# Optimization experiments

Hardware: AMD Instinct MI355X
Metric: run time of the kernel (lower is better)

The kernel has to match this reference:

```python
import jax, jax.numpy as jnp
import numpy as np

B, F, D = 32, 4096, 256
ALPHA = 0.001


def setup_inputs() -> dict:
    key = jax.random.key(0)
    ks = jax.random.split(key, 9)
    s = 1.0 / np.sqrt(D)
    return {
        "q": jax.random.normal(ks[0], (B, F, D), dtype=jnp.float32),
        "k": jax.random.normal(ks[1], (B, F, D), dtype=jnp.float32),
        "v": jax.random.normal(ks[2], (B, F, D), dtype=jnp.float32),
        "Wq": jax.random.normal(ks[3], (D, D), dtype=jnp.float32) * s,
        "bq": jax.random.normal(ks[4], (D,), dtype=jnp.float32) * 0.01,
        "Wk": jax.random.normal(ks[5], (D, D), dtype=jnp.float32) * s,
        "bk": jax.random.normal(ks[6], (D,), dtype=jnp.float32) * 0.01,
        "Wv": jax.random.normal(ks[7], (D, D), dtype=jnp.float32) * s,
        "bv": jax.random.normal(ks[8], (D,), dtype=jnp.float32) * 0.01,
    }


def reference(q, k, v, Wq, bq, Wk, bk, Wv, bv):
    # nn.Linear: x @ W.T + b
    queries = q @ Wq.T + bq            # [b, f, d]
    keys = k @ Wk.T + bk               # [b, f, d]
    values = v @ Wv.T + bv             # [b, f, d]
    # batched Gram matrix + ridge term
    key_sym = jnp.einsum("bfd,bfe->bde", keys, keys)          # [b, d, d]
    key_sym = key_sym + ALPHA * jnp.eye(D, dtype=key_sym.dtype)
    key_sym_inv = jnp.linalg.inv(key_sym)                      # [b, d, d]
    kkik = jnp.einsum("bde,bfe->bdf", key_sym_inv, keys)       # [b, d, f]
    kkikv = jnp.einsum("bdf,bfe->bde", kkik, values)           # [b, d, d]
    itn = jax.nn.softmax(kkikv, axis=2)                        # sigma=True; softmax over dim 2
    h = jnp.einsum("bfd,bde->be", queries, itn)                # [b, d]
    return h
```

## Files before the change

### kernel.cpp

```cpp
#include <hip/hip_runtime.h>
#include <math.h>

#define FDIM 4096
#define DDIM 256
#define ALPHA_R 0.001f
#define SVH (3 * 32 * 256)

typedef __attribute__((ext_vector_type(8))) short short8;
typedef __attribute__((ext_vector_type(4))) float f32x4;

__device__ __forceinline__ unsigned cvt_pk_bf16(float lo_e, float hi_e) {
  unsigned r;
  asm("v_cvt_pk_bf16_f32 %0, %1, %2" : "=v"(r) : "v"(lo_e), "v"(hi_e));
  return r;
}

__global__ __launch_bounds__(256) void gram_fused(const float* __restrict__ kg,
                                                  const float* __restrict__ vg,
                                                  const float* __restrict__ qg,
                                                  float* __restrict__ Gp0,
                                                  float* __restrict__ Gp1,
                                                  float* __restrict__ svec,
                                                  float* __restrict__ part) {
  int flat = blockIdx.x;
  int tid = threadIdx.x;

  if (flat >= 1024) {
    int cs = flat - 1024;
    int chunk = cs & 15, b = cs >> 4;
    int rg = tid >> 6, dq = tid & 63;
    const float* p = qg + ((size_t)b * FDIM + chunk * 256 + rg) * DDIM + dq * 4;
    float4 s = make_float4(0.f, 0.f, 0.f, 0.f);
    for (int i = 0; i < 64; ++i) {
      float4 t = *(const float4*)(p + (size_t)i * 4 * DDIM);
      s.x += t.x; s.y += t.y; s.z += t.z; s.w += t.w;
    }
    __shared__ __align__(16) float redq[4][64][4];
    *(float4*)&redq[rg][dq][0] = s;
    __syncthreads();
    if (rg == 0) {
      float4 a0 = *(float4*)&redq[0][dq][0];
      float4 a1 = *(float4*)&redq[1][dq][0];
      float4 a2 = *(float4*)&redq[2][dq][0];
      float4 a3 = *(float4*)&redq[3][dq][0];
      float4 t = make_float4(a0.x + a1.x + a2.x + a3.x, a0.y + a1.y + a2.y + a3.y,
                             a0.z + a1.z + a2.z + a3.z, a0.w + a1.w + a2.w + a3.w);
      *(float4*)(part + ((size_t)chunk * 32 + b) * DDIM + dq * 4) = t;
    }
    return;
  }

  int xcd = flat & 7, s = flat >> 3;
  int b = xcd * 4 + (s >> 5);
  int rem = s & 31;
  int tile = rem >> 1;
  int half = rem & 1;
  int tm = tile >> 2, tn = tile & 3;
  int mBase = tm * 64, nBase = tn * 64;
  const float* Kb = kg + (size_t)b * FDIM * DDIM;
  const float* Vb = vg + (size_t)b * FDIM * DDIM;

  __shared__ __align__(16) unsigned short Ah[64][40], Al[64][40];
  __shared__ __align__(16) unsigned short Bh[64][40], Bl[64][40];
  __shared__ __align__(16) unsigned short Ch[64][40], Cl[64][40];
  __shared__ float sred[4][68];

  int w = tid >> 6, lane = tid & 63;
  int wr = w >> 1, wc = w & 1;
  int lrow = lane & 15;
  int kof = (lane >> 4) * 8;

  const float* pA = Kb + mBase + lane;
  const float* pB = Kb + nBase + lane;
  const float* pC = Vb + nBase + lane;

  bool doK = (tn == 0), doV = (tm == 0);
  float sK = 0.f, sV = 0.f;
  int fBase = half * 2048;

  float xa[8], xb[8], xc[8];
  auto loadIter = [&](int it) {
    int f = fBase + it * 32 + w * 8;
#pragma unroll
    for (int j = 0; j < 8; ++j) {
      xa[j] = pA[(size_t)(f + j) * DDIM];
      xb[j] = pB[(size_t)(f + j) * DDIM];
      xc[j] = pC[(size_t)(f + j) * DDIM];
    }
  };
  auto stash = [&](const float* x, unsigned short (*H)[40], unsigned short (*L)[40]) {
    unsigned h0 = cvt_pk_bf16(x[0], x[1]);
    unsigned h1 = cvt_pk_bf16(x[2], x[3]);
    unsigned h2 = cvt_pk_bf16(x[4], x[5]);
    unsigned h3 = cvt_pk_bf16(x[6], x[7]);
    unsigned l0 = cvt_pk_bf16(x[0] - __uint_as_float(h0 << 16),
                              x[1] - __uint_as_float(h0 & 0xFFFF0000u));
    unsigned l1 = cvt_pk_bf16(x[2] - __uint_as_float(h1 << 16),
                              x[3] - __uint_as_float(h1 & 0xFFFF0000u));
    unsigned l2 = cvt_pk_bf16(x[4] - __uint_as_float(h2 << 16),
                              x[5] - __uint_as_float(h2 & 0xFFFF0000u));
    unsigned l3 = cvt_pk_bf16(x[6] - __uint_as_float(h3 << 16),
                              x[7] - __uint_as_float(h3 & 0xFFFF0000u));
    *(uint4*)&H[lane][w * 8] = make_uint4(h0, h1, h2, h3);
    *(uint4*)&L[lane][w * 8] = make_uint4(l0, l1, l2, l3);
  };

  f32x4 acc0[2][2], acc1[2][2];
#pragma unroll
  for (int mt = 0; mt < 2; ++mt)
#pragma unroll
    for (int nt = 0; nt < 2; ++nt) {
      acc0[mt][nt] = (f32x4){0.f, 0.f, 0.f, 0.f};
      acc1[mt][nt] = (f32x4){0.f, 0.f, 0.f, 0.f};
    }

  loadIter(0);
  for (int it = 0; it < 64; ++it) {
    __syncthreads();
    stash(xa, Ah, Al);
    stash(xb, Bh, Bl);
    stash(xc, Ch, Cl);
    if (doK) sK += ((xa[0] + xa[1]) + (xa[2] + xa[3])) + ((xa[4] + xa[5]) + (xa[6] + xa[7]));
    if (doV) sV += ((xc[0] + xc[1]) + (xc[2] + xc[3])) + ((xc[4] + xc[5]) + (xc[6] + xc[7]));
    __syncthreads();
    if (it < 63) loadIter(it + 1);

    short8 bh[2], bl[2], ch[2], cl[2];
#pragma unroll
    for (int nt = 0; nt < 2; ++nt) {
      int rB = wc * 32 + nt * 16 + lrow;
      bh[nt] = *(const short8*)&Bh[rB][kof];
      bl[nt] = *(const short8*)&Bl[rB][kof];
      ch[nt] = *(const short8*)&Ch[rB][kof];
      cl[nt] = *(const short8*)&Cl[rB][kof];
    }
    __builtin_amdgcn_s_setprio(1);
#pragma unroll
    for (int mt = 0; mt < 2; ++mt) {
      int rA = wr * 32 + mt * 16 + lrow;
      short8 ah = *(const short8*)&Ah[rA][kof];
      short8 al = *(const short8*)&Al[rA][kof];
#pragma unroll
      for (int nt = 0; nt < 2; ++nt) {
        f32x4 t = acc0[mt][nt];
        t = __builtin_amdgcn_mfma_f32_16x16x32_bf16(ah, bh[nt], t, 0, 0, 0);
        t = __builtin_amdgcn_mfma_f32_16x16x32_bf16(ah, bl[nt], t, 0, 0, 0);
        t = __builtin_amdgcn_mfma_f32_16x16x32_bf16(al, bh[nt], t, 0, 0, 0);
        acc0[mt][nt] = t;
        f32x4 u = acc1[mt][nt];
        u = __builtin_amdgcn_mfma_f32_16x16x32_bf16(ah, ch[nt], u, 0, 0, 0);
        u = __builtin_amdgcn_mfma_f32_16x16x32_bf16(ah, cl[nt], u, 0, 0, 0);
        u = __builtin_amdgcn_mfma_f32_16x16x32_bf16(al, ch[nt], u, 0, 0, 0);
        acc1[mt][nt] = u;
      }
    }
    __builtin_amdgcn_s_setprio(0);
  }

  float* Gp = half ? Gp1 : Gp0;
  float* G0 = Gp + ((size_t)b * 2) * 65536;
  float* G1 = G0 + 65536;
#pragma unroll
  for (int mt = 0; mt < 2; ++mt)
#pragma unroll
    for (int nt = 0; nt < 2; ++nt)
#pragma unroll
      for (int r = 0; r < 4; ++r) {
        int row = mBase + wr * 32 + mt * 16 + (lane >> 4) * 4 + r;
        int col = nBase + wc * 32 + nt * 16 + (lane & 15);
        G0[(size_t)row * DDIM + col] = acc0[mt][nt][r];
        G1[(size_t)row * DDIM + col] = acc1[mt][nt][r];
      }

  float* svecH = svec + (size_t)half * SVH;
  if (doK) {
    __syncthreads();
    sred[w][lane] = sK;
    __syncthreads();
    if (tid < 64) {
      float t = sred[0][tid] + sred[1][tid] + sred[2][tid] + sred[3][tid];
      svecH[(size_t)1 * 32 * 256 + (size_t)b * 256 + mBase + tid] = t;
    }
  }
  if (doV) {
    __syncthreads();
    sred[w][lane] = sV;
    __syncthreads();
    if (tid < 64) {
      float t = sred[0][tid] + sred[1][tid] + sred[2][tid] + sred[3][tid];
      svecH[(size_t)2 * 32 * 256 + (size_t)b * 256 + nBase + tid] = t;
    }
  }
}

__global__ void smallvec(const float* __restrict__ Wq, const float* __restrict__ bq,
                         const float* __restrict__ Wk, const float* __restrict__ Wv,
                         const float* __restrict__ part,
                         const float* __restrict__ svec, float* __restrict__ uvec) {
  int b = blockIdx.x; int d = threadIdx.x;
  __shared__ float sq[256], sk[256], sv[256];
  float sqv = 0.f;
  for (int c = 0; c < 16; ++c) sqv += part[((size_t)c * 32 + b) * DDIM + d];
  sq[d] = sqv;
  sk[d] = svec[((size_t)1 * 32 + b) * DDIM + d] + svec[SVH + ((size_t)1 * 32 + b) * DDIM + d];
  sv[d] = svec[((size_t)2 * 32 + b) * DDIM + d] + svec[SVH + ((size_t)2 * 32 + b) * DDIM + d];
  __syncthreads();
  float uk = 0.f, uv = 0.f, uq = 0.f;
  for (int j = 0; j < 256; j += 4) {
    float4 wk4 = *(const float4*)(Wk + (size_t)d * DDIM + j);
    float4 wv4 = *(const float4*)(Wv + (size_t)d * DDIM + j);
    float4 wq4 = *(const float4*)(Wq + (size_t)d * DDIM + j);
    uk += wk4.x * sk[j] + wk4.y * sk[j + 1] + wk4.z * sk[j + 2] + wk4.w * sk[j + 3];
    uv += wv4.x * sv[j] + wv4.y * sv[j + 1] + wv4.z * sv[j + 2] + wv4.w * sv[j + 3];
    uq += wq4.x * sq[j] + wq4.y * sq[j + 1] + wq4.z * sq[j + 2] + wq4.w * sq[j + 3];
  }
  uvec[((size_t)0 * 32 + b) * DDIM + d] = uk;
  uvec[((size_t)1 * 32 + b) * DDIM + d] = uv;
  uvec[((size_t)2 * 32 + b) * DDIM + d] = uq + 4096.f * bq[d];
}

__global__ __launch_bounds__(256) void gemm_pass1(const float* __restrict__ Wk,
                                                  const float* __restrict__ Gp0,
                                                  const float* __restrict__ Gp1,
                                                  float* __restrict__ T) {
  int tile = blockIdx.x, w = blockIdx.y, b = blockIdx.z;
  int tm = tile >> 2, tn = tile & 3;
  const float* A = Wk;
  const float* B0 = Gp0 + ((size_t)b * 2 + w) * 65536;
  const float* B1 = Gp1 + ((size_t)b * 2 + w) * 65536;
  float* C = T + ((size_t)b * 2 + w) * 65536;
  __shared__ __align__(16) float As[16][64];
  __shared__ __align__(16) float Bs[16][64];
  int tid = threadIdx.x;
  int ty = tid >> 4, tx = tid & 15;
  int am = tid & 63, ak4 = tid >> 6;
  int brow = tid >> 4, bcol4 = tid & 15;
  int mBase = tm * 64, nBase = tn * 64;
  float acc[4][4];
#pragma unroll
  for (int i = 0; i < 4; i++)
#pragma unroll
    for (int j = 0; j < 4; j++) acc[i][j] = 0.f;
  for (int k0 = 0; k0 < 256; k0 += 16) {
    float4 a = *(const float4*)(A + (size_t)(mBase + am) * DDIM + k0 + ak4 * 4);
    size_t boff = (size_t)(k0 + brow) * DDIM + nBase + bcol4 * 4;
    float4 b0 = *(const float4*)(B0 + boff);
    float4 b1 = *(const float4*)(B1 + boff);
    float4 bb = make_float4(b0.x + b1.x, b0.y + b1.y, b0.z + b1.z, b0.w + b1.w);
    __syncthreads();
    As[ak4 * 4 + 0][am] = a.x; As[ak4 * 4 + 1][am] = a.y;
    As[ak4 * 4 + 2][am] = a.z; As[ak4 * 4 + 3][am] = a.w;
    *(float4*)&Bs[brow][bcol4 * 4] = bb;
    __syncthreads();
#pragma unroll
    for (int kstep = 0; kstep < 16; ++kstep) {
      float4 a4 = *(const float4*)&As[kstep][ty * 4];
      float4 b4 = *(const float4*)&Bs[kstep][tx * 4];
      float av[4] = {a4.x, a4.y, a4.z, a4.w};
      float bvv[4] = {b4.x, b4.y, b4.z, b4.w};
#pragma unroll
      for (int i = 0; i < 4; i++)
#pragma unroll
        for (int j = 0; j < 4; j++)
          acc[i][j] = fmaf(av[i], bvv[j], acc[i][j]);
    }
  }
#pragma unroll
  for (int i = 0; i < 4; i++) {
    float4 o = make_float4(acc[i][0], acc[i][1], acc[i][2], acc[i][3]);
    *(float4*)(C + (size_t)(mBase + ty * 4 + i) * DDIM + nBase + tx * 4) = o;
  }
}

__global__ __launch_bounds__(256) void gemm_pass2(const float* __restrict__ T,
                                                  const float* __restrict__ Wk,
                                                  const float* __restrict__ Wv,
                                                  float* __restrict__ S,
                                                  const float* __restrict__ uvec,
                                                  const float* __restrict__ bk,
                                                  const float* __restrict__ bv) {
  int tile = blockIdx.x, w = blockIdx.y, b = blockIdx.z;
  int tm = tile >> 2, tn = tile & 3;
  const float* A = T + ((size_t)b * 2 + w) * 65536;
  const float* W = w ? Wv : Wk;
  float* C = S + ((size_t)b * 2 + w) * 65536;
  __shared__ __align__(16) float As[16][64];
  __shared__ __align__(16) float Bs[16][64];
  int tid = threadIdx.x;
  int ty = tid >> 4, tx = tid & 15;
  int am = tid & 63, ak4 = tid >> 6;
  int mBase = tm * 64, nBase = tn * 64;
  float acc[4][4];
#pragma unroll
  for (int i = 0; i < 4; i++)
#pragma unroll
    for (int j = 0; j < 4; j++) acc[i][j] = 0.f;
  for (int k0 = 0; k0 < 256; k0 += 16) {
    float4 a = *(const float4*)(A + (size_t)(mBase + am) * DDIM + k0 + ak4 * 4);
    float4 bb = *(const float4*)(W + (size_t)(nBase + am) * DDIM + k0 + ak4 * 4);
    __syncthreads();
    As[ak4 * 4 + 0][am] = a.x; As[ak4 * 4 + 1][am] = a.y;
    As[ak4 * 4 + 2][am] = a.z; As[ak4 * 4 + 3][am] = a.w;
    Bs[ak4 * 4 + 0][am] = bb.x; Bs[ak4 * 4 + 1][am] = bb.y;
    Bs[ak4 * 4 + 2][am] = bb.z; Bs[ak4 * 4 + 3][am] = bb.w;
    __syncthreads();
#pragma unroll
    for (int kstep = 0; kstep < 16; ++kstep) {
      float4 a4 = *(const float4*)&As[kstep][ty * 4];
      float4 b4 = *(const float4*)&Bs[kstep][tx * 4];
      float av[4] = {a4.x, a4.y, a4.z, a4.w};
      float bvv[4] = {b4.x, b4.y, b4.z, b4.w};
#pragma unroll
      for (int i = 0; i < 4; i++)
#pragma unroll
        for (int j = 0; j < 4; j++)
          acc[i][j] = fmaf(av[i], bvv[j], acc[i][j]);
    }
  }
  const float* uk = uvec + ((size_t)0 * 32 + b) * DDIM;
  const float* uvv = uvec + ((size_t)1 * 32 + b) * DDIM;
  float ukr[4], bkr[4], ue[4], be[4];
#pragma unroll
  for (int i = 0; i < 4; ++i) {
    int row = mBase + ty * 4 + i;
    ukr[i] = uk[row]; bkr[i] = bk[row];
  }
#pragma unroll
  for (int j = 0; j < 4; ++j) {
    int col = nBase + tx * 4 + j;
    ue[j] = w ? uvv[col] : uk[col];
    be[j] = w ? bv[col] : bk[col];
  }
#pragma unroll
  for (int i = 0; i < 4; i++) {
    int row = mBase + ty * 4 + i;
#pragma unroll
    for (int j = 0; j < 4; j++) {
      int col = nBase + tx * 4 + j;
      float add = ukr[i] * be[j] + bkr[i] * ue[j] + 4096.f * bkr[i] * be[j];
      if (w == 0 && row == col) add += ALPHA_R;
      acc[i][j] += add;
    }
    float4 o = make_float4(acc[i][0], acc[i][1], acc[i][2], acc[i][3]);
    *(float4*)(C + (size_t)row * DDIM + nBase + tx * 4) = o;
  }
}

__global__ __launch_bounds__(1024, 4) void gj_factor(float* __restrict__ Sb,
                                                     float* __restrict__ Mtg) {
  int b = blockIdx.x;
  float* A = Sb + (size_t)b * 2 * 65536;
  int tid = threadIdx.x;
  int r = tid >> 2;
  int q = tid & 3;

  __shared__ __align__(16) float Mt[64][264];
  __shared__ __align__(16) float Sst[64][200];
  __shared__ __align__(16) float prow[2][64];
  __shared__ float fac[2][256];

  for (int pg = 0; pg < 4; ++pg) {
    float x[16];
    {
      const float* Ar = A + (size_t)r * 256 + pg * 64 + q * 16;
#pragma unroll
      for (int m = 0; m < 4; ++m) {
        float4 t = *(const float4*)(Ar + m * 4);
        x[m * 4 + 0] = t.x; x[m * 4 + 1] = t.y;
        x[m * 4 + 2] = t.z; x[m * 4 + 3] = t.w;
      }
    }
    if (r == pg * 64) {
      *(float4*)&prow[0][q * 16 + 0]  = make_float4(x[0], x[1], x[2], x[3]);
      *(float4*)&prow[0][q * 16 + 4]  = make_float4(x[4], x[5], x[6], x[7]);
      *(float4*)&prow[0][q * 16 + 8]  = make_float4(x[8], x[9], x[10], x[11]);
      *(float4*)&prow[0][q * 16 + 12] = make_float4(x[12], x[13], x[14], x[15]);
    }
    if (q == 0) fac[0][r] = x[0];
    __syncthreads();

#pragma unroll
    for (int jo = 0; jo < 4; ++jo) {
#pragma unroll
      for (int ji = 0; ji < 16; ++ji) {
        const int j = jo * 16 + ji;
        const int p = pg * 64 + j;
        const int buf = j & 1, nb = buf ^ 1;
        float piv = fac[buf][p];
        float ip = 1.0f / piv;
        float g = fac[buf][r] * ip;
        bool diag = (r == p);
#pragma unroll
        for (int m = 0; m < 16; ++m) {
          float pv = prow[buf][q * 16 + m];
          x[m] = diag ? pv * ip : fmaf(-g, pv, x[m]);
        }
        if (q == jo) x[ji] = diag ? ip : (0.f - g);
        if (j < 63) {
          const int jn = j + 1;
          if (r == pg * 64 + jn) {
            *(float4*)&prow[nb][q * 16 + 0]  = make_float4(x[0], x[1], x[2], x[3]);
            *(float4*)&prow[nb][q * 16 + 4]  = make_float4(x[4], x[5], x[6], x[7]);
            *(float4*)&prow[nb][q * 16 + 8]  = make_float4(x[8], x[9], x[10], x[11]);
            *(float4*)&prow[nb][q * 16 + 12] = make_float4(x[12], x[13], x[14], x[15]);
          }
          if (q == (jn >> 4)) fac[nb][r] = x[jn & 15];
        }
        __syncthreads();
      }
    }
#pragma unroll
    for (int m = 0; m < 16; ++m) Mt[q * 16 + m][r] = x[m];
    __syncthreads();

    {
      int j = tid >> 4, rseg = (tid & 15) * 16;
      float* dst = Mtg + (((size_t)b * 4 + pg) * 64 + j) * 256 + rseg;
#pragma unroll
      for (int m = 0; m < 4; ++m) {
        float4 t = make_float4(Mt[j][rseg + m * 4 + 0], Mt[j][rseg + m * 4 + 1],
                               Mt[j][rseg + m * 4 + 2], Mt[j][rseg + m * 4 + 3]);
        *(float4*)(dst + m * 4) = t;
      }
    }

    int W = (3 - pg) * 64;
    if (W > 0) {
      int c_off = (pg + 1) * 64;
      {
        int cpt = W >> 4;
        int jr = tid >> 4, tc = tid & 15;
        const float* src = A + (size_t)(pg * 64 + jr) * 256 + c_off + tc * cpt;
        for (int m = 0; m < cpt; m += 4) {
          float4 t = *(const float4*)(src + m);
          *(float4*)&Sst[jr][tc * cpt + m] = t;
        }
      }
      __syncthreads();
      int colTiles = W >> 3;
      int rt = tid / colTiles;
      int ctile = tid - rt * colTiles;
      if (rt < 32) {
        int r0 = rt * 8, c0 = ctile * 8;
        float acc[8][8];
#pragma unroll
        for (int i = 0; i < 8; ++i)
#pragma unroll
          for (int j2 = 0; j2 < 8; ++j2) acc[i][j2] = 0.f;
        for (int j = 0; j < 64; ++j) {
          float4 m0 = *(const float4*)&Mt[j][r0];
          float4 m1 = *(const float4*)&Mt[j][r0 + 4];
          float4 s0 = *(const float4*)&Sst[j][c0];
          float4 s1 = *(const float4*)&Sst[j][c0 + 4];
          float mv[8] = {m0.x, m0.y, m0.z, m0.w, m1.x, m1.y, m1.z, m1.w};
          float sv[8] = {s0.x, s0.y, s0.z, s0.w, s1.x, s1.y, s1.z, s1.w};
#pragma unroll
          for (int i = 0; i < 8; ++i)
#pragma unroll
            for (int j2 = 0; j2 < 8; ++j2)
              acc[i][j2] = fmaf(mv[i], sv[j2], acc[i][j2]);
        }
#pragma unroll
        for (int ii = 0; ii < 8; ++ii) {
          int row = r0 + ii;
          bool inPanel = ((row >> 6) == pg);
          float* dst = A + (size_t)row * 256 + c_off + c0;
          float4 o0 = make_float4(acc[ii][0], acc[ii][1], acc[ii][2], acc[ii][3]);
          float4 o1 = make_float4(acc[ii][4], acc[ii][5], acc[ii][6], acc[ii][7]);
          if (!inPanel) {
            float4 a0 = *(const float4*)(dst);
            float4 a1 = *(const float4*)(dst + 4);
            o0.x += a0.x; o0.y += a0.y; o0.z += a0.z; o0.w += a0.w;
            o1.x += a1.x; o1.y += a1.y; o1.z += a1.z; o1.w += a1.w;
          }
          *(float4*)(dst) = o0;
          *(float4*)(dst + 4) = o1;
        }
      }
      __syncthreads();
    }
  }
}

__global__ __launch_bounds__(256) void gj_apply(float* __restrict__ Sb,
                                                const float* __restrict__ Mtg) {
  int blk = blockIdx.x;
  int b = blk >> 3;
  int cbase = (blk & 7) * 32;
  float* Bm = Sb + ((size_t)b * 2 + 1) * 65536;
  int tid = threadIdx.x;
  int rt = tid >> 3;
  int ct = tid & 7;

  __shared__ __align__(16) float Mt[64][260];
  __shared__ __align__(8) float Bp[64][34];

  float4 breg[8];
#pragma unroll
  for (int i = 0; i < 8; ++i)
    breg[i] = *(const float4*)(Bm + (size_t)(rt * 8 + i) * 256 + cbase + ct * 4);

  for (int pg = 0; pg < 4; ++pg) {
    __syncthreads();
    {
      int j = tid >> 2, seg = (tid & 3) * 64;
      const float* src = Mtg + (((size_t)b * 4 + pg) * 64 + j) * 256 + seg;
#pragma unroll
      for (int m = 0; m < 16; ++m) {
        float4 t = *(const float4*)(src + m * 4);
        *(float4*)&Mt[j][seg + m * 4] = t;
      }
    }
    if (rt >= pg * 8 && rt < (pg + 1) * 8) {
#pragma unroll
      for (int i = 0; i < 8; ++i) {
        int j = (rt - pg * 8) * 8 + i;
        *(float2*)&Bp[j][ct * 4]     = make_float2(breg[i].x, breg[i].y);
        *(float2*)&Bp[j][ct * 4 + 2] = make_float2(breg[i].z, breg[i].w);
      }
    }
    __syncthreads();

    float acc[8][4];
#pragma unroll
    for (int i = 0; i < 8; ++i)
#pragma unroll
      for (int c = 0; c < 4; ++c) acc[i][c] = 0.f;
#pragma unroll 4
    for (int j = 0; j < 64; ++j) {
      float4 m0 = *(const float4*)&Mt[j][rt * 8];
      float4 m1 = *(const float4*)&Mt[j][rt * 8 + 4];
      float2 b0 = *(const float2*)&Bp[j][ct * 4];
      float2 b1 = *(const float2*)&Bp[j][ct * 4 + 2];
      float mv[8] = {m0.x, m0.y, m0.z, m0.w, m1.x, m1.y, m1.z, m1.w};
      float bv4[4] = {b0.x, b0.y, b1.x, b1.y};
#pragma unroll
      for (int i = 0; i < 8; ++i)
#pragma unroll
        for (int c = 0; c < 4; ++c)
          acc[i][c] = fmaf(mv[i], bv4[c], acc[i][c]);
    }
    bool inPanel = ((rt >> 3) == pg);
#pragma unroll
    for (int i = 0; i < 8; ++i) {
      if (inPanel) {
        breg[i] = make_float4(acc[i][0], acc[i][1], acc[i][2], acc[i][3]);
      } else {
        breg[i].x += acc[i][0]; breg[i].y += acc[i][1];
        breg[i].z += acc[i][2]; breg[i].w += acc[i][3];
      }
    }
  }

#pragma unroll
  for (int i = 0; i < 8; ++i)
    *(float4*)(Bm + (size_t)(rt * 8 + i) * 256 + cbase + ct * 4) = breg[i];
}

__global__ void softmax_h(const float* __restrict__ S,
                          const float* __restrict__ uvec,
                          float* __restrict__ out) {
  int b = blockIdx.x;
  const float* X = S + ((size_t)b * 2 + 1) * 65536;
  int tid = threadIdx.x; int lane = tid & 63; int wv = tid >> 6;
  __shared__ float mrow[256], qos[256];
  __shared__ float qs_s[256];
  qs_s[tid] = uvec[((size_t)2 * 32 + b) * DDIM + tid];
  for (int rr = 0; rr < 64; ++rr) {
    int row = rr * 4 + wv;
    float x0 = X[row * 256 + lane];
    float x1 = X[row * 256 + lane + 64];
    float x2 = X[row * 256 + lane + 128];
    float x3 = X[row * 256 + lane + 192];
    float m = fmaxf(fmaxf(x0, x1), fmaxf(x2, x3));
    for (int o = 32; o > 0; o >>= 1) m = fmaxf(m, __shfl_xor(m, o, 64));
    float s = expf(x0 - m) + expf(x1 - m) + expf(x2 - m) + expf(x3 - m);
    for (int o = 32; o > 0; o >>= 1) s += __shfl_xor(s, o, 64);
    if (lane == 0) {
      mrow[row] = m;
      qos[row] = s;
    }
  }
  __syncthreads();
  qos[tid] = qs_s[tid] / qos[tid];
  __syncthreads();
  int e = tid;
  float acc = 0.f;
  for (int d = 0; d < 256; ++d)
    acc += qos[d] * expf(X[d * 256 + e] - mrow[d]);
  out[(size_t)b * 256 + e] = acc;
}

extern "C" void kernel_launch(void* const* d_in, const int* in_sizes, int n_in,
                              void* d_out, int out_size, void* d_ws, size_t ws_size,
                              hipStream_t stream) {
  const float* q  = (const float*)d_in[0];
  const float* k  = (const float*)d_in[1];
  const float* v  = (const float*)d_in[2];
  const float* Wq = (const float*)d_in[3];
  const float* bq = (const float*)d_in[4];
  const float* Wk = (const float*)d_in[5];
  const float* bk = (const float*)d_in[6];
  const float* Wv = (const float*)d_in[7];
  const float* bv = (const float*)d_in[8];
  float* out = (float*)d_out;

  float* ws   = (float*)d_ws;
  float* Gbuf = ws;
  float* Tbuf = Gbuf + (size_t)32 * 2 * 65536;
  float* Sbuf = Tbuf + (size_t)32 * 2 * 65536;
  float* part = Sbuf + (size_t)32 * 2 * 65536;
  float* svec = part + (size_t)16 * 3 * 32 * 256;
  float* uvec = svec + (size_t)2 * 3 * 32 * 256;

  gram_fused<<<1536, 256, 0, stream>>>(k, v, q, Gbuf, Sbuf, svec, part);
  smallvec<<<32, 256, 0, stream>>>(Wq, bq, Wk, Wv, part, svec, uvec);
  gemm_pass1<<<dim3(16, 2, 32), 256, 0, stream>>>(Wk, Gbuf, Sbuf, Tbuf);
  gemm_pass2<<<dim3(16, 2, 32), 256, 0, stream>>>(Tbuf, Wk, Wv, Sbuf, uvec, bk, bv);
  gj_factor<<<32, 1024, 0, stream>>>(Sbuf, Gbuf);
  gj_apply<<<256, 256, 0, stream>>>(Sbuf, Gbuf);
  softmax_h<<<32, 256, 0, stream>>>(Sbuf, uvec, out);
}
```

Before: 515.4 us.

## Factor panel with one row per thread using 256-thread blocks

The Gauss-Jordan panel factorization now gives each of 256 threads a full 64-column row segment in registers instead of splitting each row across 4 threads in a 1024-thread block. The pivot factor is taken from the thread's own register, so the shared fac array and its writes go away. Barriers now synchronize 4 waves instead of 16, which should cut per-pivot synchronization cost in the 64-step serial loop. In exchange each thread does 4x more serial FMAs per pivot and holds 64 live floats, and the trailing-update GEMM is spread over fewer threads using strided loops.

Measured after the change: 1.438 ms. 179% more time.

```diff
diff --git a/kernel.cpp b/kernel.cpp
--- a/kernel.cpp
+++ b/kernel.cpp
@@ -346,102 +346,88 @@
   }
 }
 
-__global__ __launch_bounds__(1024, 4) void gj_factor(float* __restrict__ Sb,
-                                                     float* __restrict__ Mtg) {
+__global__ __launch_bounds__(256, 1) void gj_factor(float* __restrict__ Sb,
+                                                    float* __restrict__ Mtg) {
   int b = blockIdx.x;
   float* A = Sb + (size_t)b * 2 * 65536;
   int tid = threadIdx.x;
-  int r = tid >> 2;
-  int q = tid & 3;
 
   __shared__ __align__(16) float Mt[64][264];
   __shared__ __align__(16) float Sst[64][200];
   __shared__ __align__(16) float prow[2][64];
-  __shared__ float fac[2][256];
 
   for (int pg = 0; pg < 4; ++pg) {
-    float x[16];
+    int pg64 = pg * 64;
+    float x[64];
     {
-      const float* Ar = A + (size_t)r * 256 + pg * 64 + q * 16;
-#pragma unroll
-      for (int m = 0; m < 4; ++m) {
-        float4 t = *(const float4*)(Ar + m * 4);
-        x[m * 4 + 0] = t.x; x[m * 4 + 1] = t.y;
-        x[m * 4 + 2] = t.z; x[m * 4 + 3] = t.w;
-      }
-    }
-    if (r == pg * 64) {
-      *(float4*)&prow[0][q * 16 + 0]  = make_float4(x[0], x[1], x[2], x[3]);
-      *(float4*)&prow[0][q * 16 + 4]  = make_float4(x[4], x[5], x[6], x[7]);
-      *(float4*)&prow[0][q * 16 + 8]  = make_float4(x[8], x[9], x[10], x[11]);
-      *(float4*)&prow[0][q * 16 + 12] = make_float4(x[12], x[13], x[14], x[15]);
-    }
-    if (q == 0) fac[0][r] = x[0];
-    __syncthreads();
-
-#pragma unroll
-    for (int jo = 0; jo < 4; ++jo) {
-#pragma unroll
-      for (int ji = 0; ji < 16; ++ji) {
-        const int j = jo * 16 + ji;
-        const int p = pg * 64 + j;
-        const int buf = j & 1, nb = buf ^ 1;
-        float piv = fac[buf][p];
-        float ip = 1.0f / piv;
-        float g = fac[buf][r] * ip;
-        bool diag = (r == p);
-#pragma unroll
-        for (int m = 0; m < 16; ++m) {
-          float pv = prow[buf][q * 16 + m];
-          x[m] = diag ? pv * ip : fmaf(-g, pv, x[m]);
-        }
-        if (q == jo) x[ji] = diag ? ip : (0.f - g);
-        if (j < 63) {
-          const int jn = j + 1;
-          if (r == pg * 64 + jn) {
-            *(float4*)&prow[nb][q * 16 + 0]  = make_float4(x[0], x[1], x[2], x[3]);
-            *(float4*)&prow[nb][q * 16 + 4]  = make_float4(x[4], x[5], x[6], x[7]);
-            *(float4*)&prow[nb][q * 16 + 8]  = make_float4(x[8], x[9], x[10], x[11]);
-            *(float4*)&prow[nb][q * 16 + 12] = make_float4(x[12], x[13], x[14], x[15]);
-          }
-          if (q == (jn >> 4)) fac[nb][r] = x[jn & 15];
-        }
-        __syncthreads();
-      }
-    }
-#pragma unroll
-    for (int m = 0; m < 16; ++m) Mt[q * 16 + m][r] = x[m];
+      const float* Ar = A + (size_t)tid * 256 + pg64;
+#pragma unroll
+      for (int m4 = 0; m4 < 16; ++m4) {
+        float4 t = *(const float4*)(Ar + m4 * 4);
+        x[m4 * 4 + 0] = t.x; x[m4 * 4 + 1] = t.y;
+        x[m4 * 4 + 2] = t.z; x[m4 * 4 + 3] = t.w;
+      }
+    }
+    if (tid == pg64) {
+#pragma unroll
+      for (int m4 = 0; m4 < 16; ++m4)
+        *(float4*)&prow[0][m4 * 4] =
+            make_float4(x[m4 * 4], x[m4 * 4 + 1], x[m4 * 4 + 2], x[m4 * 4 + 3]);
+    }
+    __syncthreads();
+
+#pragma unroll
+    for (int j = 0; j < 64; ++j) {
+      const int buf = j & 1, nb = buf ^ 1;
+      float pj = prow[buf][j];
+      float ip = 1.0f / pj;
+      bool diag = (tid == pg64 + j);
+      if (diag) {
+#pragma unroll
+        for (int m = 0; m < 64; ++m) x[m] = prow[buf][m] * ip;
+        x[j] = ip;
+      } else {
+        float g = x[j] * ip;
+#pragma unroll
+        for (int m = 0; m < 64; ++m) x[m] = fmaf(-g, prow[buf][m], x[m]);
+        x[j] = 0.f - g;
+      }
+      if (j < 63 && tid == pg64 + j + 1) {
+#pragma unroll
+        for (int m4 = 0; m4 < 16; ++m4)
+          *(float4*)&prow[nb][m4 * 4] =
+              make_float4(x[m4 * 4], x[m4 * 4 + 1], x[m4 * 4 + 2], x[m4 * 4 + 3]);
+      }
+      __syncthreads();
+    }
+
+#pragma unroll
+    for (int j = 0; j < 64; ++j) Mt[j][tid] = x[j];
     __syncthreads();
 
     {
-      int j = tid >> 4, rseg = (tid & 15) * 16;
-      float* dst = Mtg + (((size_t)b * 4 + pg) * 64 + j) * 256 + rseg;
-#pragma unroll
-      for (int m = 0; m < 4; ++m) {
-        float4 t = make_float4(Mt[j][rseg + m * 4 + 0], Mt[j][rseg + m * 4 + 1],
-                               Mt[j][rseg + m * 4 + 2], Mt[j][rseg + m * 4 + 3]);
-        *(float4*)(dst + m * 4) = t;
-      }
+      int j = tid >> 2, seg = (tid & 3) * 64;
+      float* dst = Mtg + (((size_t)b * 4 + pg) * 64 + j) * 256 + seg;
+#pragma unroll
+      for (int m = 0; m < 16; ++m)
+        *(float4*)(dst + m * 4) = *(const float4*)&Mt[j][seg + m * 4];
     }
 
     int W = (3 - pg) * 64;
     if (W > 0) {
-      int c_off = (pg + 1) * 64;
-      {
-        int cpt = W >> 4;
-        int jr = tid >> 4, tc = tid & 15;
-        const float* src = A + (size_t)(pg * 64 + jr) * 256 + c_off + tc * cpt;
-        for (int m = 0; m < cpt; m += 4) {
-          float4 t = *(const float4*)(src + m);
-          *(float4*)&Sst[jr][tc * cpt + m] = t;
-        }
+      int c_off = pg64 + 64;
+      int W4 = W >> 2;
+      for (int t = tid; t < 64 * W4; t += 256) {
+        int j = t / W4, cq = t - j * W4;
+        float4 v2 = *(const float4*)(A + (size_t)(pg64 + j) * 256 + c_off + cq * 4);
+        *(float4*)&Sst[j][cq * 4] = v2;
       }
       __syncthreads();
-      int colTiles = W >> 3;
-      int rt = tid / colTiles;
-      int ctile = tid - rt * colTiles;
-      if (rt < 32) {
-        int r0 = rt * 8, c0 = ctile * 8;
+      int colT = W >> 3;
+      int nT = 32 * colT;
+      for (int t = tid; t < nT; t += 256) {
+        int rt = t / colT, ct = t - rt * colT;
+        int r0 = rt * 8, c0 = ct * 8;
         float acc[8][8];
 #pragma unroll
         for (int i = 0; i < 8; ++i)
@@ -477,8 +463,8 @@
           *(float4*)(dst + 4) = o1;
         }
       }
-      __syncthreads();
-    }
+    }
+    __syncthreads();
   }
 }
 
@@ -617,7 +603,7 @@
   smallvec<<<32, 256, 0, stream>>>(Wq, bq, Wk, Wv, part, svec, uvec);
   gemm_pass1<<<dim3(16, 2, 32), 256, 0, stream>>>(Wk, Gbuf, Sbuf, Tbuf);
   gemm_pass2<<<dim3(16, 2, 32), 256, 0, stream>>>(Tbuf, Wk, Wv, Sbuf, uvec, bk, bv);
-  gj_factor<<<32, 1024, 0, stream>>>(Sbuf, Gbuf);
+  gj_factor<<<32, 256, 0, stream>>>(Sbuf, Gbuf);
   gj_apply<<<256, 256, 0, stream>>>(Sbuf, Gbuf);
   softmax_h<<<32, 256, 0, stream>>>(Sbuf, uvec, out);
 }
```

## Move projection GEMM passes to split-bf16 MFMA with register prefetch

Applied to the files above, without the earlier changes.

Rewrites gemm_pass1 and gemm_pass2, which compute the weight-sandwiched Gram products, from scalar FP32 FMA tiles to MFMA 16x16x32 bf16 instructions. Each FP32 operand is split into high and low bf16 parts, and three MFMAs per tile approximate FP32 precision. Global loads for the next K-slice are prefetched into registers while MFMAs run, and a shared hilo8 helper replaces the inline split code. The aim is to cut the ALU cost of these 32x2 batched 256^3 GEMMs. The trade-off is small precision loss from dropping the lo*lo term and uncoalesced column-strided B loads in pass1.

Measured after the change: 483.6 us. 1.07x faster.

```diff
diff --git a/kernel.cpp b/kernel.cpp
--- a/kernel.cpp
+++ b/kernel.cpp
@@ -13,6 +13,23 @@
   unsigned r;
   asm("v_cvt_pk_bf16_f32 %0, %1, %2" : "=v"(r) : "v"(lo_e), "v"(hi_e));
   return r;
+}
+
+__device__ __forceinline__ void hilo8(const float* x, uint4& H, uint4& L) {
+  unsigned h0 = cvt_pk_bf16(x[0], x[1]);
+  unsigned h1 = cvt_pk_bf16(x[2], x[3]);
+  unsigned h2 = cvt_pk_bf16(x[4], x[5]);
+  unsigned h3 = cvt_pk_bf16(x[6], x[7]);
+  unsigned l0 = cvt_pk_bf16(x[0] - __uint_as_float(h0 << 16),
+                            x[1] - __uint_as_float(h0 & 0xFFFF0000u));
+  unsigned l1 = cvt_pk_bf16(x[2] - __uint_as_float(h1 << 16),
+                            x[3] - __uint_as_float(h1 & 0xFFFF0000u));
+  unsigned l2 = cvt_pk_bf16(x[4] - __uint_as_float(h2 << 16),
+                            x[5] - __uint_as_float(h2 & 0xFFFF0000u));
+  unsigned l3 = cvt_pk_bf16(x[6] - __uint_as_float(h3 << 16),
+                            x[7] - __uint_as_float(h3 & 0xFFFF0000u));
+  H = make_uint4(h0, h1, h2, h3);
+  L = make_uint4(l0, l1, l2, l3);
 }
 
 __global__ __launch_bounds__(256) void gram_fused(const float* __restrict__ kg,
@@ -89,20 +106,10 @@
     }
   };
   auto stash = [&](const float* x, unsigned short (*H)[40], unsigned short (*L)[40]) {
-    unsigned h0 = cvt_pk_bf16(x[0], x[1]);
-    unsigned h1 = cvt_pk_bf16(x[2], x[3]);
-    unsigned h2 = cvt_pk_bf16(x[4], x[5]);
-    unsigned h3 = cvt_pk_bf16(x[6], x[7]);
-    unsigned l0 = cvt_pk_bf16(x[0] - __uint_as_float(h0 << 16),
-                              x[1] - __uint_as_float(h0 & 0xFFFF0000u));
-    unsigned l1 = cvt_pk_bf16(x[2] - __uint_as_float(h1 << 16),
-                              x[3] - __uint_as_float(h1 & 0xFFFF0000u));
-    unsigned l2 = cvt_pk_bf16(x[4] - __uint_as_float(h2 << 16),
-                              x[5] - __uint_as_float(h2 & 0xFFFF0000u));
-    unsigned l3 = cvt_pk_bf16(x[6] - __uint_as_float(h3 << 16),
-                              x[7] - __uint_as_float(h3 & 0xFFFF0000u));
-    *(uint4*)&H[lane][w * 8] = make_uint4(h0, h1, h2, h3);
-    *(uint4*)&L[lane][w * 8] = make_uint4(l0, l1, l2, l3);
+    uint4 hh, ll;
+    hilo8(x, hh, ll);
+    *(uint4*)&H[lane][w * 8] = hh;
+    *(uint4*)&L[lane][w * 8] = ll;
   };
 
   f32x4 acc0[2][2], acc1[2][2];
@@ -223,53 +230,97 @@
                                                   const float* __restrict__ Gp0,
                                                   const float* __restrict__ Gp1,
                                                   float* __restrict__ T) {
-  int tile = blockIdx.x, w = blockIdx.y, b = blockIdx.z;
+  int tile = blockIdx.x, wsel = blockIdx.y, b = blockIdx.z;
   int tm = tile >> 2, tn = tile & 3;
+  int mBase = tm * 64, nBase = tn * 64;
   const float* A = Wk;
-  const float* B0 = Gp0 + ((size_t)b * 2 + w) * 65536;
-  const float* B1 = Gp1 + ((size_t)b * 2 + w) * 65536;
-  float* C = T + ((size_t)b * 2 + w) * 65536;
-  __shared__ __align__(16) float As[16][64];
-  __shared__ __align__(16) float Bs[16][64];
+  const float* B0 = Gp0 + ((size_t)b * 2 + wsel) * 65536;
+  const float* B1 = Gp1 + ((size_t)b * 2 + wsel) * 65536;
+  float* C = T + ((size_t)b * 2 + wsel) * 65536;
+
+  __shared__ __align__(16) unsigned short Ah[64][40], Al[64][40];
+  __shared__ __align__(16) unsigned short Bh[64][40], Bl[64][40];
+
   int tid = threadIdx.x;
-  int ty = tid >> 4, tx = tid & 15;
-  int am = tid & 63, ak4 = tid >> 6;
-  int brow = tid >> 4, bcol4 = tid & 15;
-  int mBase = tm * 64, nBase = tn * 64;
-  float acc[4][4];
-#pragma unroll
-  for (int i = 0; i < 4; i++)
-#pragma unroll
-    for (int j = 0; j < 4; j++) acc[i][j] = 0.f;
-  for (int k0 = 0; k0 < 256; k0 += 16) {
-    float4 a = *(const float4*)(A + (size_t)(mBase + am) * DDIM + k0 + ak4 * 4);
-    size_t boff = (size_t)(k0 + brow) * DDIM + nBase + bcol4 * 4;
-    float4 b0 = *(const float4*)(B0 + boff);
-    float4 b1 = *(const float4*)(B1 + boff);
-    float4 bb = make_float4(b0.x + b1.x, b0.y + b1.y, b0.z + b1.z, b0.w + b1.w);
-    __syncthreads();
-    As[ak4 * 4 + 0][am] = a.x; As[ak4 * 4 + 1][am] = a.y;
-    As[ak4 * 4 + 2][am] = a.z; As[ak4 * 4 + 3][am] = a.w;
-    *(float4*)&Bs[brow][bcol4 * 4] = bb;
-    __syncthreads();
-#pragma unroll
-    for (int kstep = 0; kstep < 16; ++kstep) {
-      float4 a4 = *(const float4*)&As[kstep][ty * 4];
-      float4 b4 = *(const float4*)&Bs[kstep][tx * 4];
-      float av[4] = {a4.x, a4.y, a4.z, a4.w};
-      float bvv[4] = {b4.x, b4.y, b4.z, b4.w};
-#pragma unroll
-      for (int i = 0; i < 4; i++)
-#pragma unroll
-        for (int j = 0; j < 4; j++)
-          acc[i][j] = fmaf(av[i], bvv[j], acc[i][j]);
-    }
-  }
-#pragma unroll
-  for (int i = 0; i < 4; i++) {
-    float4 o = make_float4(acc[i][0], acc[i][1], acc[i][2], acc[i][3]);
-    *(float4*)(C + (size_t)(mBase + ty * 4 + i) * DDIM + nBase + tx * 4) = o;
-  }
+  int w = tid >> 6, lane = tid & 63;
+  int wr = w >> 1, wc = w & 1;
+  int lrow = lane & 15;
+  int kof = (lane >> 4) * 8;
+  int ar = tid >> 2, aq = tid & 3;
+  const float* pArow = A + (size_t)(mBase + ar) * DDIM + aq * 8;
+  int bw = tid >> 6;
+  const float* pB0 = B0 + nBase + lane;
+  const float* pB1 = B1 + nBase + lane;
+
+  float xa[8], xb[8];
+  auto loadIter = [&](int k0) {
+    float4 a0 = *(const float4*)(pArow + k0);
+    float4 a1 = *(const float4*)(pArow + k0 + 4);
+    xa[0] = a0.x; xa[1] = a0.y; xa[2] = a0.z; xa[3] = a0.w;
+    xa[4] = a1.x; xa[5] = a1.y; xa[6] = a1.z; xa[7] = a1.w;
+#pragma unroll
+    for (int j = 0; j < 8; ++j) {
+      size_t o = (size_t)(k0 + bw * 8 + j) * DDIM;
+      xb[j] = pB0[o] + pB1[o];
+    }
+  };
+
+  f32x4 acc[2][2];
+#pragma unroll
+  for (int mt = 0; mt < 2; ++mt)
+#pragma unroll
+    for (int nt = 0; nt < 2; ++nt) acc[mt][nt] = (f32x4){0.f, 0.f, 0.f, 0.f};
+
+  loadIter(0);
+  for (int it = 0; it < 8; ++it) {
+    __syncthreads();
+    {
+      uint4 hh, ll;
+      hilo8(xa, hh, ll);
+      *(uint4*)&Ah[ar][aq * 8] = hh;
+      *(uint4*)&Al[ar][aq * 8] = ll;
+      hilo8(xb, hh, ll);
+      *(uint4*)&Bh[lane][bw * 8] = hh;
+      *(uint4*)&Bl[lane][bw * 8] = ll;
+    }
+    __syncthreads();
+    if (it < 7) loadIter((it + 1) * 32);
+
+    short8 bh[2], bl[2];
+#pragma unroll
+    for (int nt = 0; nt < 2; ++nt) {
+      int rB = wc * 32 + nt * 16 + lrow;
+      bh[nt] = *(const short8*)&Bh[rB][kof];
+      bl[nt] = *(const short8*)&Bl[rB][kof];
+    }
+    __builtin_amdgcn_s_setprio(1);
+#pragma unroll
+    for (int mt = 0; mt < 2; ++mt) {
+      int rA = wr * 32 + mt * 16 + lrow;
+      short8 ah = *(const short8*)&Ah[rA][kof];
+      short8 al = *(const short8*)&Al[rA][kof];
+#pragma unroll
+      for (int nt = 0; nt < 2; ++nt) {
+        f32x4 t = acc[mt][nt];
+        t = __builtin_amdgcn_mfma_f32_16x16x32_bf16(ah, bh[nt], t, 0, 0, 0);
+        t = __builtin_amdgcn_mfma_f32_16x16x32_bf16(ah, bl[nt], t, 0, 0, 0);
+        t = __builtin_amdgcn_mfma_f32_16x16x32_bf16(al, bh[nt], t, 0, 0, 0);
+        acc[mt][nt] = t;
+      }
+    }
+    __builtin_amdgcn_s_setprio(0);
+  }
+
+#pragma unroll
+  for (int mt = 0; mt < 2; ++mt)
+#pragma unroll
+    for (int nt = 0; nt < 2; ++nt)
+#pragma unroll
+      for (int r = 0; r < 4; ++r) {
+        int row = mBase + wr * 32 + mt * 16 + (lane >> 4) * 4 + r;
+        int col = nBase + wc * 32 + nt * 16 + (lane & 15);
+        C[(size_t)row * DDIM + col] = acc[mt][nt][r];
+      }
 }
 
 __global__ __launch_bounds__(256) void gemm_pass2(const float* __restrict__ T,
@@ -279,71 +330,100 @@
                                                   const float* __restrict__ uvec,
                                                   const float* __restrict__ bk,
                                                   const float* __restrict__ bv) {
-  int tile = blockIdx.x, w = blockIdx.y, b = blockIdx.z;
+  int tile = blockIdx.x, wsel = blockIdx.y, b = blockIdx.z;
   int tm = tile >> 2, tn = tile & 3;
-  const float* A = T + ((size_t)b * 2 + w) * 65536;
-  const float* W = w ? Wv : Wk;
-  float* C = S + ((size_t)b * 2 + w) * 65536;
-  __shared__ __align__(16) float As[16][64];
-  __shared__ __align__(16) float Bs[16][64];
+  int mBase = tm * 64, nBase = tn * 64;
+  const float* A = T + ((size_t)b * 2 + wsel) * 65536;
+  const float* W = wsel ? Wv : Wk;
+  float* C = S + ((size_t)b * 2 + wsel) * 65536;
+
+  __shared__ __align__(16) unsigned short Ah[64][40], Al[64][40];
+  __shared__ __align__(16) unsigned short Bh[64][40], Bl[64][40];
+
   int tid = threadIdx.x;
-  int ty = tid >> 4, tx = tid & 15;
-  int am = tid & 63, ak4 = tid >> 6;
-  int mBase = tm * 64, nBase = tn * 64;
-  float acc[4][4];
-#pragma unroll
-  for (int i = 0; i < 4; i++)
-#pragma unroll
-    for (int j = 0; j < 4; j++) acc[i][j] = 0.f;
-  for (int k0 = 0; k0 < 256; k0 += 16) {
-    float4 a = *(const float4*)(A + (size_t)(mBase + am) * DDIM + k0 + ak4 * 4);
-    float4 bb = *(const float4*)(W + (size_t)(nBase + am) * DDIM + k0 + ak4 * 4);
-    __syncthreads();
-    As[ak4 * 4 + 0][am] = a.x; As[ak4 * 4 + 1][am] = a.y;
-    As[ak4 * 4 + 2][am] = a.z; As[ak4 * 4 + 3][am] = a.w;
-    Bs[ak4 * 4 + 0][am] = bb.x; Bs[ak4 * 4 + 1][am] = bb.y;
-    Bs[ak4 * 4 + 2][am] = bb.z; Bs[ak4 * 4 + 3][am] = bb.w;
-    __syncthreads();
-#pragma unroll
-    for (int kstep = 0; kstep < 16; ++kstep) {
-      float4 a4 = *(const float4*)&As[kstep][ty * 4];
-      float4 b4 = *(const float4*)&Bs[kstep][tx * 4];
-      float av[4] = {a4.x, a4.y, a4.z, a4.w};
-      float bvv[4] = {b4.x, b4.y, b4.z, b4.w};
-#pragma unroll
-      for (int i = 0; i < 4; i++)
-#pragma unroll
-        for (int j = 0; j < 4; j++)
-          acc[i][j] = fmaf(av[i], bvv[j], acc[i][j]);
-    }
-  }
+  int w = tid >> 6, lane = tid & 63;
+  int wr = w >> 1, wc = w & 1;
+  int lrow = lane & 15;
+  int kof = (lane >> 4) * 8;
+  int ar = tid >> 2, aq = tid & 3;
+  const float* pArow = A + (size_t)(mBase + ar) * DDIM + aq * 8;
+  const float* pBrow = W + (size_t)(nBase + ar) * DDIM + aq * 8;
+
+  float xa[8], xb[8];
+  auto loadIter = [&](int k0) {
+    float4 a0 = *(const float4*)(pArow + k0);
+    float4 a1 = *(const float4*)(pArow + k0 + 4);
+    xa[0] = a0.x; xa[1] = a0.y; xa[2] = a0.z; xa[3] = a0.w;
+    xa[4] = a1.x; xa[5] = a1.y; xa[6] = a1.z; xa[7] = a1.w;
+    float4 b0 = *(const float4*)(pBrow + k0);
+    float4 b1 = *(const float4*)(pBrow + k0 + 4);
+    xb[0] = b0.x; xb[1] = b0.y; xb[2] = b0.z; xb[3] = b0.w;
+    xb[4] = b1.x; xb[5] = b1.y; xb[6] = b1.z; xb[7] = b1.w;
+  };
+
+  f32x4 acc[2][2];
+#pragma unroll
+  for (int mt = 0; mt < 2; ++mt)
+#pragma unroll
+    for (int nt = 0; nt < 2; ++nt) acc[mt][nt] = (f32x4){0.f, 0.f, 0.f, 0.f};
+
+  loadIter(0);
+  for (int it = 0; it < 8; ++it) {
+    __syncthreads();
+    {
+      uint4 hh, ll;
+      hilo8(xa, hh, ll);
+      *(uint4*)&Ah[ar][aq * 8] = hh;
+      *(uint4*)&Al[ar][aq * 8] = ll;
+      hilo8(xb, hh, ll);
+      *(uint4*)&Bh[ar][aq * 8] = hh;
+      *(uint4*)&Bl[ar][aq * 8] = ll;
+    }
+    __syncthreads();
+    if (it < 7) loadIter((it + 1) * 32);
+
+    short8 bh[2], bl[2];
+#pragma unroll
+    for (int nt = 0; nt < 2; ++nt) {
+      int rB = wc * 32 + nt * 16 + lrow;
+      bh[nt] = *(const short8*)&Bh[rB][kof];
+      bl[nt] = *(const short8*)&Bl[rB][kof];
+    }
+    __builtin_amdgcn_s_setprio(1);
+#pragma unroll
+    for (int mt = 0; mt < 2; ++mt) {
+      int rA = wr * 32 + mt * 16 + lrow;
+      short8 ah = *(const short8*)&Ah[rA][kof];
+      short8 al = *(const short8*)&Al[rA][kof];
+#pragma unroll
+      for (int nt = 0; nt < 2; ++nt) {
+        f32x4 t = acc[mt][nt];
+        t = __builtin_amdgcn_mfma_f32_16x16x32_bf16(ah, bh[nt], t, 0, 0, 0);
+        t = __builtin_amdgcn_mfma_f32_16x16x32_bf16(ah, bl[nt], t, 0, 0, 0);
+        t = __builtin_amdgcn_mfma_f32_16x16x32_bf16(al, bh[nt], t, 0, 0, 0);
+        acc[mt][nt] = t;
+      }
+    }
+    __builtin_amdgcn_s_setprio(0);
+  }
+
   const float* uk = uvec + ((size_t)0 * 32 + b) * DDIM;
   const float* uvv = uvec + ((size_t)1 * 32 + b) * DDIM;
-  float ukr[4], bkr[4], ue[4], be[4];
-#pragma unroll
-  for (int i = 0; i < 4; ++i) {
-    int row = mBase + ty * 4 + i;
-    ukr[i] = uk[row]; bkr[i] = bk[row];
-  }
-#pragma unroll
-  for (int j = 0; j < 4; ++j) {
-    int col = nBase + tx * 4 + j;
-    ue[j] = w ? uvv[col] : uk[col];
-    be[j] = w ? bv[col] : bk[col];
-  }
-#pragma unroll
-  for (int i = 0; i < 4; i++) {
-    int row = mBase + ty * 4 + i;
-#pragma unroll
-    for (int j = 0; j < 4; j++) {
-      int col = nBase + tx * 4 + j;
-      float add = ukr[i] * be[j] + bkr[i] * ue[j] + 4096.f * bkr[i] * be[j];
-      if (w == 0 && row == col) add += ALPHA_R;
-      acc[i][j] += add;
-    }
-    float4 o = make_float4(acc[i][0], acc[i][1], acc[i][2], acc[i][3]);
-    *(float4*)(C + (size_t)row * DDIM + nBase + tx * 4) = o;
-  }
+#pragma unroll
+  for (int mt = 0; mt < 2; ++mt)
+#pragma unroll
+    for (int nt = 0; nt < 2; ++nt) {
+      int col = nBase + wc * 32 + nt * 16 + (lane & 15);
+      float ue = wsel ? uvv[col] : uk[col];
+      float be = wsel ? bv[col] : bk[col];
+#pragma unroll
+      for (int r = 0; r < 4; ++r) {
+        int row = mBase + wr * 32 + mt * 16 + (lane >> 4) * 4 + r;
+        float add = uk[row] * be + bk[row] * ue + 4096.f * bk[row] * be;
+        if (wsel == 0 && row == col) add += ALPHA_R;
+        C[(size_t)row * DDIM + col] = acc[mt][nt][r] + add;
+      }
+    }
 }
 
 __global__ __launch_bounds__(1024, 4) void gj_factor(float* __restrict__ Sb,
```
